# Kernel optimization log

Measured on AMD Instinct MI355X. Metric: run time of the kernel, lower is better.

## Reference

```python
import jax, jax.numpy as jnp
import numpy as np

B, T, C, D = 4, 20, 128, 64
TD = T * D  # 1280; adaptor input dim = 2*TD = 2560


def setup_inputs() -> dict:
    key = jax.random.key(0)
    ks = jax.random.split(key, 12)

    def lin(k, out_d, in_d):
        return jax.random.normal(k, (out_d, in_d), jnp.float32) / np.float32(np.sqrt(in_d))

    return {
        "h": jax.random.normal(ks[0], (B, T, C, D), jnp.float32),
        "W1": lin(ks[1], 128, 2 * TD), "b1": jnp.zeros((128,), jnp.float32),
        "W2": lin(ks[2], 256, 128),   "b2": jnp.zeros((256,), jnp.float32),
        "W3": lin(ks[3], 64, 256),    "b3": jnp.zeros((64,), jnp.float32),
        "W4": lin(ks[4], 1, 64),      "b4": jnp.zeros((1,), jnp.float32),
        "A_a": jax.random.normal(ks[5], (C, C), jnp.float32) * 0.01,
        "A_m": jax.random.normal(ks[6], (C, C), jnp.float32) * 0.01,
        "W_add": lin(ks[7], D, D), "b_add": jnp.zeros((D,), jnp.float32),
        "W_mod": lin(ks[8], D, D), "b_mod": jnp.zeros((D,), jnp.float32),
        "beta1": jnp.float32(1.0), "beta2": jnp.float32(1.0), "beta3": jnp.float32(1.0),
    }


def reference(h, W1, b1, W2, b2, W3, b3, W4, b4, A_a, A_m,
              W_add, b_add, W_mod, b_mod, beta1, beta2, beta3):
    Bb, Tt, Cc, Dd = h.shape
    td = Tt * Dd
    # H^(u) flattened over time: (B, C, T*D)
    h_flat = jnp.transpose(h, (0, 2, 1, 3)).reshape(Bb, Cc, td)

    # Adaptor MLP on concat(H^u, H^v). First layer is linear on the concat,
    # so split W1 and broadcast-add instead of materializing (B,C,C,2*T*D).
    W1u, W1v = W1[:, :td], W1[:, td:]
    fu = h_flat @ W1u.T                      # (B, C, 128) contribution of u
    fv = h_flat @ W1v.T                      # (B, C, 128) contribution of v
    x = jax.nn.relu(fu[:, :, None, :] + fv[:, None, :, :] + b1)   # (B, Cu, Cv, 128)
    x = jax.nn.relu(jnp.einsum('buvk,mk->buvm', x, W2) + b2)       # (B, Cu, Cv, 256)
    x = jax.nn.relu(jnp.einsum('buvk,mk->buvm', x, W3) + b3)       # (B, Cu, Cv, 64)
    s = jax.nn.sigmoid(jnp.einsum('buvk,mk->buvm', x, W4) + b4)[..., 0]  # (B, C, C)

    # Add path: a_t^(v) = sum_u S^(u,v) * A_a^(u,v) * h_t^(u)
    w = s * A_a[None]                        # (B, Cu, Cv)
    a = jnp.einsum('buv,btud->btvd', w, h)   # (B, T, C, D)
    a = a @ W_add.T + b_add

    # Modulator path: m_t^(v) = (sum_u A_m^(u,v) h_t^(u)) * h_t^(v)
    m = jnp.einsum('uv,btud->btvd', A_m, h) * h
    m = m @ W_mod.T + b_mod

    return beta1 * h + beta2 * a + beta3 * m
```

## Files before the change

kernel.cpp:

```cpp
#include <hip/hip_runtime.h>
#include <cmath>

#define NB 4
#define NT 20
#define NC 128
#define ND 64
#define TD 1280

typedef short short8 __attribute__((ext_vector_type(8)));
typedef float f32x4 __attribute__((ext_vector_type(4)));

static __device__ __forceinline__ unsigned short f2bf(float f) {
  union { float f; unsigned int u; } v; v.f = f;
  unsigned int r = v.u + 0x7FFFu + ((v.u >> 16) & 1u);
  return (unsigned short)(r >> 16);
}

static __device__ __forceinline__ void conv16(const float* __restrict__ s,
                                              unsigned short* __restrict__ d) {
#pragma unroll
  for (int q = 0; q < 2; q++) {
    float4 f0 = *(const float4*)(s + q * 8);
    float4 f1 = *(const float4*)(s + q * 8 + 4);
    uint4 o;
    o.x = (unsigned)f2bf(f0.x) | ((unsigned)f2bf(f0.y) << 16);
    o.y = (unsigned)f2bf(f0.z) | ((unsigned)f2bf(f0.w) << 16);
    o.z = (unsigned)f2bf(f1.x) | ((unsigned)f2bf(f1.y) << 16);
    o.w = (unsigned)f2bf(f1.z) | ((unsigned)f2bf(f1.w) << 16);
    *(uint4*)(d + q * 8) = o;
  }
}

__global__ __launch_bounds__(256) void k_conv_a(
    const float* __restrict__ h, const float* __restrict__ W1,
    unsigned short* __restrict__ hbf, unsigned short* __restrict__ W1bf) {
  int blk = blockIdx.x, tid = threadIdx.x;
  if (blk < 160) {
    int bt = blk >> 1;
    int j = ((blk & 1) << 12) + tid * 16;
    int b = bt / 20;
    int c = j >> 6, d0 = j & 63;
    int t5 = bt - b * 20;
    conv16(h + (size_t)bt * 8192 + j,
           hbf + ((size_t)(b * NC + c)) * TD + t5 * 64 + d0);
  } else {
    size_t i = (size_t)(blk - 160) * 4096 + tid * 16;
    conv16(W1 + i, W1bf + i);
  }
}

__global__ __launch_bounds__(128) void k_fuv2(
    const unsigned short* __restrict__ hbf,
    const unsigned short* __restrict__ W1bf,
    const float* __restrict__ h, const float* __restrict__ W2,
    const float* __restrict__ W3, const float* __restrict__ A_m,
    const float* __restrict__ W_add, const float* __restrict__ W_mod,
    float* __restrict__ fuv,
    unsigned short* __restrict__ W2bf, unsigned short* __restrict__ W3bf,
    unsigned short* __restrict__ A_mTbf, unsigned short* __restrict__ W_addbf,
    unsigned short* __restrict__ W_modbf, unsigned short* __restrict__ hbfT) {
  __shared__ float hsl[128][65];
  int blk = blockIdx.x, tid = threadIdx.x;
  if (blk < 256) {
    int mtile = blk & 15;
    int ntile = blk >> 4;
    int lane = tid & 63;
    int w = tid >> 6;
    int lr = lane & 15, lhi = lane >> 4;
    int row = mtile * 32 + w * 16 + lr;
    const unsigned short* ap = hbf + (size_t)row * TD + lhi * 8;
    int n = ntile * 16 + lr;
    const unsigned short* bp =
        W1bf + (size_t)(n & 127) * (2 * TD) + (n >> 7) * TD + lhi * 8;
    f32x4 acc = (f32x4){0.f, 0.f, 0.f, 0.f};
#pragma unroll 4
    for (int kb = 0; kb < TD; kb += 32) {
      short8 a = *(const short8*)(ap + kb);
      short8 bv = *(const short8*)(bp + kb);
      acc = __builtin_amdgcn_mfma_f32_16x16x32_bf16(a, bv, acc, 0, 0, 0);
    }
    int m0 = mtile * 32 + w * 16 + lhi * 4;
#pragma unroll
    for (int r = 0; r < 4; r++)
      fuv[(size_t)(m0 + r) * 256 + n] = acc[r];
    return;
  }
  int cb = blk - 256;
  if (cb < 16) {
    size_t i = (size_t)cb * 2048 + tid * 16;
    conv16(W2 + i, W2bf + i);
  } else if (cb < 24) {
    size_t i = (size_t)(cb - 16) * 2048 + tid * 16;
    conv16(W3 + i, W3bf + i);
  } else if (cb < 32) {
    size_t base = (size_t)(cb - 24) * 2048 + tid * 16;
    unsigned short tmp[16];
#pragma unroll
    for (int i2 = 0; i2 < 16; i2++) {
      size_t idx = base + i2;
      int v = (int)(idx >> 7), u = (int)(idx & 127);
      tmp[i2] = f2bf(A_m[(size_t)u * 128 + v]);
    }
    *(uint4*)(A_mTbf + base) = *(uint4*)tmp;
    *(uint4*)(A_mTbf + base + 8) = *(uint4*)(tmp + 8);
  } else if (cb < 34) {
    size_t i = (size_t)(cb - 32) * 2048 + tid * 16;
    conv16(W_add + i, W_addbf + i);
  } else if (cb < 36) {
    size_t i = (size_t)(cb - 34) * 2048 + tid * 16;
    conv16(W_mod + i, W_modbf + i);
  } else {
    int bt = cb - 36;
    const float* hb = h + (size_t)bt * 8192;
    for (int i = tid; i < 8192; i += 128) hsl[i >> 6][i & 63] = hb[i];
    __syncthreads();
    unsigned short* ob = hbfT + (size_t)bt * 8192;
    for (int i = tid; i < 8192; i += 128) {
      int d = i >> 7, u = i & 127;
      ob[i] = f2bf(hsl[u][d]);
    }
  }
}

__global__ __launch_bounds__(256) void k_pair(
    const float* __restrict__ fuv, const float* __restrict__ b1,
    const unsigned short* __restrict__ W2bf, const float* __restrict__ b2,
    const unsigned short* __restrict__ W3bf, const float* __restrict__ b3,
    const float* __restrict__ W4, const float* __restrict__ b4,
    const float* __restrict__ A_a, unsigned short* __restrict__ wTbf) {
  int blk = blockIdx.x;
  int b = blk >> 7;
  int u = blk & 127;
  __shared__ char x1raw[32768];
  __shared__ char ycraw[4][4096];
  __shared__ char w2c[16384];
  __shared__ char w3c[8192];
  int t = threadIdx.x;
  int lane = t & 63;
  int w = t >> 6;
  const float* fub = fuv + ((size_t)(b * NC + u)) * 256;

  for (int s = w; s < 16; s += 4) {
    int o = s * 1024 + lane * 16;
    int row = o >> 8;
    int cbo = o & 255;
    const char* src = (const char*)W2bf + (size_t)row * 256 +
                      (cbo ^ ((row & 7) << 4));
    __builtin_amdgcn_global_load_lds(src, w2c + s * 1024, 16, 0, 0);
  }
  for (int s = w; s < 8; s += 4) {
    int o = s * 1024 + lane * 16;
    int row = o >> 7;
    int cbo = o & 127;
    const char* src = (const char*)W3bf + (size_t)row * 512 +
                      (cbo ^ ((row & 7) << 4));
    __builtin_amdgcn_global_load_lds(src, w3c + s * 1024, 16, 0, 0);
  }

  {
    int v = t >> 1;
    int kh2 = (t & 1) << 6;
    const float* fvrow = fuv + ((size_t)(b * NC + v)) * 256 + 128 + kh2;
    const float* fur = fub + kh2;
    const float* b1r = b1 + kh2;
    int swv = (v & 7) << 4;
    int rowbase = v * 256 + kh2 * 2;
    for (int kc = 0; kc < 64; kc += 8) {
      float e[8];
#pragma unroll
      for (int i2 = 0; i2 < 8; i2++) {
        float val = fur[kc + i2] + fvrow[kc + i2] + b1r[kc + i2];
        e[i2] = val > 0.f ? val : 0.f;
      }
      unsigned int pw[4];
#pragma unroll
      for (int i2 = 0; i2 < 4; i2++)
        pw[i2] = (unsigned int)f2bf(e[2 * i2]) |
                 ((unsigned int)f2bf(e[2 * i2 + 1]) << 16);
      *(uint4*)(x1raw + ((rowbase + kc * 2) ^ swv)) =
          make_uint4(pw[0], pw[1], pw[2], pw[3]);
    }
  }
  __syncthreads();

  int v0w = w * 32;
  int lr = lane & 15;
  int lhi = lane >> 4;
  int sw = (lr & 7) << 4;
  char* ycb = ycraw[w];
  f32x4 zacc[2][4];
#pragma unroll
  for (int q = 0; q < 2; q++)
#pragma unroll
    for (int n = 0; n < 4; n++) zacc[q][n] = (f32x4){0.f, 0.f, 0.f, 0.f};

  for (int mc = 0; mc < 256; mc += 64) {
    if (mc) {
      __syncthreads();
      for (int s = w; s < 16; s += 4) {
        int o = s * 1024 + lane * 16;
        int row = o >> 8;
        int cbo = o & 255;
        const char* src = (const char*)W2bf + (size_t)(mc + row) * 256 +
                          (cbo ^ ((row & 7) << 4));
        __builtin_amdgcn_global_load_lds(src, w2c + s * 1024, 16, 0, 0);
      }
      for (int s = w; s < 8; s += 4) {
        int o = s * 1024 + lane * 16;
        int row = o >> 7;
        int cbo = o & 127;
        const char* src = (const char*)W3bf + (size_t)row * 512 + mc * 2 +
                          (cbo ^ ((row & 7) << 4));
        __builtin_amdgcn_global_load_lds(src, w3c + s * 1024, 16, 0, 0);
      }
      __syncthreads();
    }

    f32x4 yac[4][2];
#pragma unroll
    for (int mt = 0; mt < 4; mt++) {
      yac[mt][0] = (f32x4){0.f, 0.f, 0.f, 0.f};
      yac[mt][1] = (f32x4){0.f, 0.f, 0.f, 0.f};
    }
#pragma unroll
    for (int ks = 0; ks < 4; ks++) {
      int kb = ks * 32 + lhi * 8;
      int r0 = (v0w + lr) * 256 + kb * 2;
      short8 x0 = *(const short8*)(x1raw + (r0 ^ sw));
      short8 x1v = *(const short8*)(x1raw + ((r0 + 16 * 256) ^ sw));
#pragma unroll
      for (int mt = 0; mt < 4; mt++) {
        int wrow = mt * 16 + lr;
        short8 wv = *(const short8*)(
            w2c + wrow * 256 + ((ks * 64 + lhi * 16) ^ ((wrow & 7) << 4)));
        yac[mt][0] = __builtin_amdgcn_mfma_f32_16x16x32_bf16(wv, x0, yac[mt][0], 0, 0, 0);
        yac[mt][1] = __builtin_amdgcn_mfma_f32_16x16x32_bf16(wv, x1v, yac[mt][1], 0, 0, 0);
      }
    }
#pragma unroll
    for (int mt = 0; mt < 4; mt++) {
      float4 b2v = *(const float4*)(b2 + mc + mt * 16 + lhi * 4);
#pragma unroll
      for (int vg = 0; vg < 2; vg++) {
        int v = vg * 16 + lr;
        float e0 = yac[mt][vg][0] + b2v.x; e0 = e0 > 0.f ? e0 : 0.f;
        float e1 = yac[mt][vg][1] + b2v.y; e1 = e1 > 0.f ? e1 : 0.f;
        float e2 = yac[mt][vg][2] + b2v.z; e2 = e2 > 0.f ? e2 : 0.f;
        float e3 = yac[mt][vg][3] + b2v.w; e3 = e3 > 0.f ? e3 : 0.f;
        uint2 pw;
        pw.x = (unsigned)f2bf(e0) | ((unsigned)f2bf(e1) << 16);
        pw.y = (unsigned)f2bf(e2) | ((unsigned)f2bf(e3) << 16);
        int byte = (v * 128 + (mt * 16 + lhi * 4) * 2) ^ ((lr & 7) << 4);
        *(uint2*)(ycb + byte) = pw;
      }
    }
#pragma unroll
    for (int ks2 = 0; ks2 < 2; ks2++) {
      int kb = ks2 * 32 + lhi * 8;
      short8 ya0 = *(const short8*)(ycb + ((lr * 128 + kb * 2) ^ sw));
      short8 ya1 = *(const short8*)(ycb + (((16 + lr) * 128 + kb * 2) ^ sw));
#pragma unroll
      for (int n = 0; n < 4; n++) {
        int jrow = 16 * n + lr;
        short8 w3v = *(const short8*)(
            w3c + jrow * 128 + ((ks2 * 64 + lhi * 16) ^ ((jrow & 7) << 4)));
        zacc[0][n] = __builtin_amdgcn_mfma_f32_16x16x32_bf16(ya0, w3v, zacc[0][n], 0, 0, 0);
        zacc[1][n] = __builtin_amdgcn_mfma_f32_16x16x32_bf16(ya1, w3v, zacc[1][n], 0, 0, 0);
      }
    }
  }

  float sp[2][4];
#pragma unroll
  for (int q = 0; q < 2; q++)
#pragma unroll
    for (int r = 0; r < 4; r++) sp[q][r] = 0.f;
#pragma unroll
  for (int n = 0; n < 4; n++) {
    int j = 16 * n + lr;
    float b3v = b3[j], w4v = W4[j];
#pragma unroll
    for (int q = 0; q < 2; q++)
#pragma unroll
      for (int r = 0; r < 4; r++) {
        float z = zacc[q][n][r] + b3v;
        z = z > 0.f ? z : 0.f;
        sp[q][r] += w4v * z;
      }
  }
#pragma unroll
  for (int mask = 1; mask <= 8; mask <<= 1)
#pragma unroll
    for (int q = 0; q < 2; q++)
#pragma unroll
      for (int r = 0; r < 4; r++)
        sp[q][r] += __shfl_xor(sp[q][r], mask, 64);
  float bb4 = b4[0];
  if (lr == 0) {
#pragma unroll
    for (int q = 0; q < 2; q++)
#pragma unroll
      for (int r = 0; r < 4; r++) {
        int v = v0w + 16 * q + lhi * 4 + r;
        float s = 1.f / (1.f + expf(-(sp[q][r] + bb4)));
        wTbf[((size_t)(b * NC + v)) * NC + u] = f2bf(s * A_a[u * NC + v]);
      }
  }
}

__global__ __launch_bounds__(64) void k_out_mfma(
    const float* __restrict__ h, const unsigned short* __restrict__ wTbf,
    const unsigned short* __restrict__ A_mTbf,
    const unsigned short* __restrict__ hbfT,
    const unsigned short* __restrict__ W_addbf,
    const unsigned short* __restrict__ W_modbf,
    const float* __restrict__ b_add, const float* __restrict__ b_mod,
    const float* __restrict__ beta1p, const float* __restrict__ beta2p,
    const float* __restrict__ beta3p, float* __restrict__ out) {
  int blk = blockIdx.x;
  int bt = blk >> 3;
  int v0 = (blk & 7) << 4;
  int b = bt / 20;
  __shared__ char apre_l[2048];
  __shared__ char mpre_l[2048];
  int lane = threadIdx.x;
  int lr = lane & 15, lhi = lane >> 4;
  f32x4 aacc[4], macc[4];
#pragma unroll
  for (int nf = 0; nf < 4; nf++) {
    aacc[nf] = (f32x4){0.f, 0.f, 0.f, 0.f};
    macc[nf] = (f32x4){0.f, 0.f, 0.f, 0.f};
  }
  const unsigned short* wrow = wTbf + ((size_t)(b * NC + v0 + lr)) * NC + lhi * 8;
  const unsigned short* arow = A_mTbf + (size_t)(v0 + lr) * NC + lhi * 8;
  const unsigned short* hTrow = hbfT + (size_t)bt * 8192 + lhi * 8;
#pragma unroll
  for (int kb = 0; kb < 128; kb += 32) {
    short8 aw = *(const short8*)(wrow + kb);
    short8 am = *(const short8*)(arow + kb);
#pragma unroll
    for (int nf = 0; nf < 4; nf++) {
      short8 bv = *(const short8*)(hTrow + (size_t)(nf * 16 + lr) * NC + kb);
      aacc[nf] = __builtin_amdgcn_mfma_f32_16x16x32_bf16(aw, bv, aacc[nf], 0, 0, 0);
      macc[nf] = __builtin_amdgcn_mfma_f32_16x16x32_bf16(am, bv, macc[nf], 0, 0, 0);
    }
  }
  float hval[4][4];
  const float* hbase = h + (size_t)bt * 8192;
#pragma unroll
  for (int nf = 0; nf < 4; nf++) {
    int d = nf * 16 + lr;
#pragma unroll
    for (int r = 0; r < 4; r++) {
      int vl = lhi * 4 + r;
      float hv = hbase[(size_t)(v0 + vl) * 64 + d];
      hval[nf][r] = hv;
      int byte = (vl * 128 + d * 2) ^ ((vl & 7) << 4);
      *(unsigned short*)(apre_l + byte) = f2bf(aacc[nf][r]);
      *(unsigned short*)(mpre_l + byte) = f2bf(macc[nf][r] * hv);
    }
  }
  f32x4 oa[4], om[4];
#pragma unroll
  for (int nf = 0; nf < 4; nf++) {
    oa[nf] = (f32x4){0.f, 0.f, 0.f, 0.f};
    om[nf] = (f32x4){0.f, 0.f, 0.f, 0.f};
  }
  int sw = (lr & 7) << 4;
#pragma unroll
  for (int kb = 0; kb < 64; kb += 32) {
    int off0 = lr * 128 + kb * 2 + lhi * 16;
    short8 pa = *(const short8*)(apre_l + (off0 ^ sw));
    short8 pm = *(const short8*)(mpre_l + (off0 ^ sw));
#pragma unroll
    for (int nf = 0; nf < 4; nf++) {
      const unsigned short* wa = W_addbf + (size_t)(nf * 16 + lr) * 64 + kb + lhi * 8;
      const unsigned short* wm = W_modbf + (size_t)(nf * 16 + lr) * 64 + kb + lhi * 8;
      short8 wav = *(const short8*)wa;
      short8 wmv = *(const short8*)wm;
      oa[nf] = __builtin_amdgcn_mfma_f32_16x16x32_bf16(pa, wav, oa[nf], 0, 0, 0);
      om[nf] = __builtin_amdgcn_mfma_f32_16x16x32_bf16(pm, wmv, om[nf], 0, 0, 0);
    }
  }
  float bb1 = beta1p[0], bb2 = beta2p[0], bb3 = beta3p[0];
  float* obase = out + (size_t)bt * 8192 + (size_t)v0 * 64;
#pragma unroll
  for (int nf = 0; nf < 4; nf++) {
    int d = nf * 16 + lr;
    float ba = b_add[d], bm = b_mod[d];
#pragma unroll
    for (int r = 0; r < 4; r++) {
      int vl = lhi * 4 + r;
      obase[(size_t)vl * 64 + d] =
          bb1 * hval[nf][r] + bb2 * (oa[nf][r] + ba) + bb3 * (om[nf][r] + bm);
    }
  }
}

extern "C" void kernel_launch(void* const* d_in, const int* in_sizes, int n_in,
                              void* d_out, int out_size, void* d_ws, size_t ws_size,
                              hipStream_t stream) {
  const float* h     = (const float*)d_in[0];
  const float* W1    = (const float*)d_in[1];
  const float* b1    = (const float*)d_in[2];
  const float* W2    = (const float*)d_in[3];
  const float* b2    = (const float*)d_in[4];
  const float* W3    = (const float*)d_in[5];
  const float* b3    = (const float*)d_in[6];
  const float* W4    = (const float*)d_in[7];
  const float* b4    = (const float*)d_in[8];
  const float* A_a   = (const float*)d_in[9];
  const float* A_m   = (const float*)d_in[10];
  const float* W_add = (const float*)d_in[11];
  const float* b_add = (const float*)d_in[12];
  const float* W_mod = (const float*)d_in[13];
  const float* b_mod = (const float*)d_in[14];
  const float* beta1 = (const float*)d_in[15];
  const float* beta2 = (const float*)d_in[16];
  const float* beta3 = (const float*)d_in[17];
  float* out = (float*)d_out;

  char* ws = (char*)d_ws;
  float* fuv             = (float*)(ws);
  unsigned short* wTbf   = (unsigned short*)(ws + 512 * 1024);
  unsigned short* A_mTbf = (unsigned short*)(ws + 640 * 1024);
  unsigned short* W_addbf= (unsigned short*)(ws + 672 * 1024);
  unsigned short* W_modbf= (unsigned short*)(ws + 680 * 1024);
  unsigned short* W2bf   = (unsigned short*)(ws + 688 * 1024);
  unsigned short* W3bf   = (unsigned short*)(ws + 752 * 1024);
  unsigned short* W1bf   = (unsigned short*)(ws + 784 * 1024);
  unsigned short* hbf    = (unsigned short*)(ws + 1424 * 1024);
  unsigned short* hbfT   = (unsigned short*)(ws + 2704 * 1024);

  k_conv_a<<<240, 256, 0, stream>>>(h, W1, hbf, W1bf);
  k_fuv2<<<372, 128, 0, stream>>>(hbf, W1bf, h, W2, W3, A_m, W_add, W_mod,
                                  fuv, W2bf, W3bf, A_mTbf, W_addbf, W_modbf,
                                  hbfT);
  k_pair<<<512, 256, 0, stream>>>(fuv, b1, W2bf, b2, W3bf, b3, W4, b4, A_a, wTbf);
  k_out_mfma<<<640, 64, 0, stream>>>(h, wTbf, A_mTbf, hbfT, W_addbf, W_modbf,
                                     b_add, b_mod, beta1, beta2, beta3, out);
}
```

Baseline: 45.69 us.

## Keep layer-1 activations in registers and double-buffer W2/W3 chunk loads

The first-layer ReLU outputs are now computed straight into MFMA operand registers instead of being staged through a 32KB shared buffer. The W2/W3 weight chunks are double-buffered, so the next chunk is prefetched with global_load_lds while the current one feeds the MFMAs. This leaves one barrier per chunk instead of two. The aim is to hide weight-load latency, remove the LDS round trip for activations, and cut LDS use to allow more resident blocks. In exchange, register pressure rises and each fuv row is read redundantly per wave.

Result: faster. 43.66 us (-4.4%).

```diff
diff --git a/kernel.cpp b/kernel.cpp
--- a/kernel.cpp
+++ b/kernel.cpp
@@ -131,14 +131,16 @@
   int blk = blockIdx.x;
   int b = blk >> 7;
   int u = blk & 127;
-  __shared__ char x1raw[32768];
   __shared__ char ycraw[4][4096];
-  __shared__ char w2c[16384];
-  __shared__ char w3c[8192];
+  __shared__ char w2c[2][16384];
+  __shared__ char w3c[2][8192];
   int t = threadIdx.x;
   int lane = t & 63;
   int w = t >> 6;
-  const float* fub = fuv + ((size_t)(b * NC + u)) * 256;
+  int lr = lane & 15;
+  int lhi = lane >> 4;
+  int v0w = w * 32;
+  int sw = (lr & 7) << 4;
 
   for (int s = w; s < 16; s += 4) {
     int o = s * 1024 + lane * 16;
@@ -146,7 +148,7 @@
     int cbo = o & 255;
     const char* src = (const char*)W2bf + (size_t)row * 256 +
                       (cbo ^ ((row & 7) << 4));
-    __builtin_amdgcn_global_load_lds(src, w2c + s * 1024, 16, 0, 0);
+    __builtin_amdgcn_global_load_lds(src, w2c[0] + s * 1024, 16, 0, 0);
   }
   for (int s = w; s < 8; s += 4) {
     int o = s * 1024 + lane * 16;
@@ -154,39 +156,43 @@
     int cbo = o & 127;
     const char* src = (const char*)W3bf + (size_t)row * 512 +
                       (cbo ^ ((row & 7) << 4));
-    __builtin_amdgcn_global_load_lds(src, w3c + s * 1024, 16, 0, 0);
-  }
-
+    __builtin_amdgcn_global_load_lds(src, w3c[0] + s * 1024, 16, 0, 0);
+  }
+
+  short8 xf[4][2];
   {
-    int v = t >> 1;
-    int kh2 = (t & 1) << 6;
-    const float* fvrow = fuv + ((size_t)(b * NC + v)) * 256 + 128 + kh2;
-    const float* fur = fub + kh2;
-    const float* b1r = b1 + kh2;
-    int swv = (v & 7) << 4;
-    int rowbase = v * 256 + kh2 * 2;
-    for (int kc = 0; kc < 64; kc += 8) {
-      float e[8];
-#pragma unroll
-      for (int i2 = 0; i2 < 8; i2++) {
-        float val = fur[kc + i2] + fvrow[kc + i2] + b1r[kc + i2];
-        e[i2] = val > 0.f ? val : 0.f;
-      }
-      unsigned int pw[4];
-#pragma unroll
-      for (int i2 = 0; i2 < 4; i2++)
-        pw[i2] = (unsigned int)f2bf(e[2 * i2]) |
-                 ((unsigned int)f2bf(e[2 * i2 + 1]) << 16);
-      *(uint4*)(x1raw + ((rowbase + kc * 2) ^ swv)) =
-          make_uint4(pw[0], pw[1], pw[2], pw[3]);
+    const float* fu_base = fuv + ((size_t)(b * NC + u)) * 256;
+#pragma unroll
+    for (int ks = 0; ks < 4; ks++) {
+      int k0 = ks * 32 + lhi * 8;
+      float4 fua = *(const float4*)(fu_base + k0);
+      float4 fub4 = *(const float4*)(fu_base + k0 + 4);
+      float4 b1a = *(const float4*)(b1 + k0);
+      float4 b1b = *(const float4*)(b1 + k0 + 4);
+#pragma unroll
+      for (int vg = 0; vg < 2; vg++) {
+        int v = v0w + vg * 16 + lr;
+        const float* fvr = fuv + ((size_t)(b * NC + v)) * 256 + 128 + k0;
+        float4 fva = *(const float4*)(fvr);
+        float4 fvb = *(const float4*)(fvr + 4);
+        float e[8];
+        e[0] = fua.x + fva.x + b1a.x; e[1] = fua.y + fva.y + b1a.y;
+        e[2] = fua.z + fva.z + b1a.z; e[3] = fua.w + fva.w + b1a.w;
+        e[4] = fub4.x + fvb.x + b1b.x; e[5] = fub4.y + fvb.y + b1b.y;
+        e[6] = fub4.z + fvb.z + b1b.z; e[7] = fub4.w + fvb.w + b1b.w;
+        union { unsigned int pw[4]; short8 s8; } pk;
+#pragma unroll
+        for (int i2 = 0; i2 < 4; i2++) {
+          float lo = e[2 * i2] > 0.f ? e[2 * i2] : 0.f;
+          float hi = e[2 * i2 + 1] > 0.f ? e[2 * i2 + 1] : 0.f;
+          pk.pw[i2] = (unsigned int)f2bf(lo) | ((unsigned int)f2bf(hi) << 16);
+        }
+        xf[ks][vg] = pk.s8;
+      }
     }
   }
   __syncthreads();
 
-  int v0w = w * 32;
-  int lr = lane & 15;
-  int lhi = lane >> 4;
-  int sw = (lr & 7) << 4;
   char* ycb = ycraw[w];
   f32x4 zacc[2][4];
 #pragma unroll
@@ -194,26 +200,30 @@
 #pragma unroll
     for (int n = 0; n < 4; n++) zacc[q][n] = (f32x4){0.f, 0.f, 0.f, 0.f};
 
-  for (int mc = 0; mc < 256; mc += 64) {
-    if (mc) {
-      __syncthreads();
+  for (int c = 0; c < 4; c++) {
+    int mc = c * 64;
+    char* w2cur = w2c[c & 1];
+    char* w3cur = w3c[c & 1];
+    if (c < 3) {
+      int mn = mc + 64;
+      char* w2nxt = w2c[(c + 1) & 1];
+      char* w3nxt = w3c[(c + 1) & 1];
       for (int s = w; s < 16; s += 4) {
         int o = s * 1024 + lane * 16;
         int row = o >> 8;
         int cbo = o & 255;
-        const char* src = (const char*)W2bf + (size_t)(mc + row) * 256 +
+        const char* src = (const char*)W2bf + (size_t)(mn + row) * 256 +
                           (cbo ^ ((row & 7) << 4));
-        __builtin_amdgcn_global_load_lds(src, w2c + s * 1024, 16, 0, 0);
+        __builtin_amdgcn_global_load_lds(src, w2nxt + s * 1024, 16, 0, 0);
       }
       for (int s = w; s < 8; s += 4) {
         int o = s * 1024 + lane * 16;
         int row = o >> 7;
         int cbo = o & 127;
-        const char* src = (const char*)W3bf + (size_t)row * 512 + mc * 2 +
+        const char* src = (const char*)W3bf + (size_t)row * 512 + mn * 2 +
                           (cbo ^ ((row & 7) << 4));
-        __builtin_amdgcn_global_load_lds(src, w3c + s * 1024, 16, 0, 0);
-      }
-      __syncthreads();
+        __builtin_amdgcn_global_load_lds(src, w3nxt + s * 1024, 16, 0, 0);
+      }
     }
 
     f32x4 yac[4][2];
@@ -224,17 +234,13 @@
     }
 #pragma unroll
     for (int ks = 0; ks < 4; ks++) {
-      int kb = ks * 32 + lhi * 8;
-      int r0 = (v0w + lr) * 256 + kb * 2;
-      short8 x0 = *(const short8*)(x1raw + (r0 ^ sw));
-      short8 x1v = *(const short8*)(x1raw + ((r0 + 16 * 256) ^ sw));
 #pragma unroll
       for (int mt = 0; mt < 4; mt++) {
         int wrow = mt * 16 + lr;
         short8 wv = *(const short8*)(
-            w2c + wrow * 256 + ((ks * 64 + lhi * 16) ^ ((wrow & 7) << 4)));
-        yac[mt][0] = __builtin_amdgcn_mfma_f32_16x16x32_bf16(wv, x0, yac[mt][0], 0, 0, 0);
-        yac[mt][1] = __builtin_amdgcn_mfma_f32_16x16x32_bf16(wv, x1v, yac[mt][1], 0, 0, 0);
+            w2cur + wrow * 256 + ((ks * 64 + lhi * 16) ^ ((wrow & 7) << 4)));
+        yac[mt][0] = __builtin_amdgcn_mfma_f32_16x16x32_bf16(wv, xf[ks][0], yac[mt][0], 0, 0, 0);
+        yac[mt][1] = __builtin_amdgcn_mfma_f32_16x16x32_bf16(wv, xf[ks][1], yac[mt][1], 0, 0, 0);
       }
     }
 #pragma unroll
@@ -263,11 +269,12 @@
       for (int n = 0; n < 4; n++) {
         int jrow = 16 * n + lr;
         short8 w3v = *(const short8*)(
-            w3c + jrow * 128 + ((ks2 * 64 + lhi * 16) ^ ((jrow & 7) << 4)));
+            w3cur + jrow * 128 + ((ks2 * 64 + lhi * 16) ^ ((jrow & 7) << 4)));
         zacc[0][n] = __builtin_amdgcn_mfma_f32_16x16x32_bf16(ya0, w3v, zacc[0][n], 0, 0, 0);
         zacc[1][n] = __builtin_amdgcn_mfma_f32_16x16x32_bf16(ya1, w3v, zacc[1][n], 0, 0, 0);
       }
     }
+    __syncthreads();
   }
 
   float sp[2][4];
```
